# Kernel optimization log

Measured on AMD Instinct MI355X. Metric: run time of the kernel, lower is better.

## Reference

```python
import jax, jax.numpy as jnp
import numpy as np

T, B, F_, H, D, C = 16, 1024, 512, 128, 8, 100  # trees, batch, feat, hidden, depth, classes
L = 2 ** (D + 1)  # n_leaf = 512


def _routing_tables():
    # Static per-leaf routing: node index and branch side at each depth.
    # Derived from compute_mu's gather indices:
    #   node(d, l) = 2^d - 1 + l // 2^(D+1-d);  side(d, l) = (l // 2^(D-d)) % 2
    l = np.arange(L)
    node = np.stack([(2 ** d - 1) + l // (2 ** (D + 1 - d)) for d in range(D + 1)])  # [D+1, L]
    side = np.stack([(l // (2 ** (D - d))) % 2 for d in range(D + 1)])               # [D+1, L]
    return jnp.asarray(node, dtype=jnp.int32), jnp.asarray(side.astype(np.bool_))


def setup_inputs() -> dict:
    key = jax.random.key(0)
    ks = jax.random.split(key, 4)
    return {
        "feat": jax.random.normal(ks[0], (B, F_), jnp.float32),
        "W1": jax.random.normal(ks[1], (T, F_, H), jnp.float32) * 0.05,
        "b1": jnp.zeros((T, H), jnp.float32),
        "W2": jax.random.normal(ks[2], (T, H, L), jnp.float32) * 0.05,
        "b2": jnp.zeros((T, L), jnp.float32),
        "pi": jax.random.uniform(ks[3], (T, L, C), jnp.float32, -2.0, 2.0),
    }


def reference(feat, W1, b1, W2, b2, pi):
    node, side = _routing_tables()
    # Per-tree MLP head (dropout is identity in eval mode).
    h = jax.nn.relu(jnp.einsum('bf,tfh->tbh', feat, W1) + b1[:, None, :])        # [T,B,H]
    p = jax.nn.sigmoid(jnp.einsum('tbh,thl->tbl', h, W2) + b2[:, None, :])       # [T,B,L]
    # compute_mu: product of routing probs along each root->leaf path.
    sel = p[:, :, node]                          # [T,B,D+1,L] gather (static indices)
    route = jnp.where(side, 1.0 - sel, sel)      # left -> p, right -> 1-p
    mu = jnp.prod(route, axis=2)                 # [T,B,L]
    # compute_py_x: mean over leaves then mean over trees of mu @ softmax(pi).
    leaf_p = jax.nn.softmax(pi, axis=-1)         # [T,L,C]
    py_x = jnp.einsum('tbl,tlc->bc', mu, leaf_p) / (L * T)  # [B,C]
    return jnp.log(py_x)
```

## Files before the change

### kernel.cpp

```cpp
#include <hip/hip_runtime.h>
#include <hip/hip_bf16.h>
#include <math.h>

#define T_ 16
#define B_ 1024
#define F_ 512
#define H_ 128
#define D_ 8
#define C_ 100
#define L_ 512
#define CP_ 112

typedef __attribute__((ext_vector_type(8))) short bf16x8_t;
typedef __attribute__((ext_vector_type(4))) float f32x4_t;

__device__ inline ushort f2bf(float x) {
  __hip_bfloat16 b = __float2bfloat16(x);
  return *(ushort*)&b;
}
__device__ inline float bf2f(ushort u) {
  union { unsigned int i; float f; } v;
  v.i = ((unsigned int)u) << 16;
  return v.f;
}

__device__ inline void bar_raw() {
  asm volatile("" ::: "memory");
  __builtin_amdgcn_s_barrier();
  asm volatile("" ::: "memory");
}
__device__ inline void bar_publish_lds() {
  asm volatile("s_waitcnt lgkmcnt(0)" ::: "memory");
  __builtin_amdgcn_s_barrier();
  asm volatile("" ::: "memory");
}

__global__ __launch_bounds__(256) void k_prep(
    const float* __restrict__ feat, const float* __restrict__ W1,
    const float* __restrict__ W2, const float* __restrict__ pi,
    ushort* __restrict__ feat_bf, ushort* __restrict__ W1T,
    ushort* __restrict__ W2T, ushort* __restrict__ lpT) {
  __shared__ ushort ubuf[112 * 48];
  float (*tile)[33] = (float(*)[33])ubuf;
  ushort (*tileT)[48] = (ushort(*)[48])ubuf;
  const int bid = blockIdx.x, tid = threadIdx.x;

  if (bid < 256) {
    int i = (bid * 256 + tid) * 8;
    float4 a = *(const float4*)(feat + i);
    float4 b = *(const float4*)(feat + i + 4);
    bf16x8_t o;
    o[0] = (short)f2bf(a.x); o[1] = (short)f2bf(a.y);
    o[2] = (short)f2bf(a.z); o[3] = (short)f2bf(a.w);
    o[4] = (short)f2bf(b.x); o[5] = (short)f2bf(b.y);
    o[6] = (short)f2bf(b.z); o[7] = (short)f2bf(b.w);
    *(bf16x8_t*)(feat_bf + i) = o;
    return;
  }
  if (bid < 2304) {
    const float* X; ushort* XT; int K, N, kb, nb, s;
    if (bid < 1280) {
      int r = bid - 256;  kb = r & 15; nb = (r >> 4) & 3;  s = r >> 6;
      X = W1; XT = W1T; K = F_; N = H_;
    } else {
      int r = bid - 1280; kb = r & 3;  nb = (r >> 2) & 15; s = r >> 6;
      X = W2; XT = W2T; K = H_; N = L_;
    }
    const int k0 = kb * 32, n0 = nb * 32;
    const int c = tid & 31, r0 = tid >> 5;
    const float* Xs = X + (size_t)s * K * N;
    ushort* XTs = XT + (size_t)s * N * K;
#pragma unroll
    for (int j = 0; j < 4; ++j)
      tile[r0 + 8 * j][c] = Xs[(size_t)(k0 + r0 + 8 * j) * N + n0 + c];
    __syncthreads();
#pragma unroll
    for (int j = 0; j < 4; ++j)
      XTs[(size_t)(n0 + r0 + 8 * j) * K + k0 + c] = f2bf(tile[c][r0 + 8 * j]);
    return;
  }
  {
    int bid2 = bid - 2304;
    int t = bid2 >> 4, l0 = (bid2 & 15) << 5;
    int lane = tid & 63;
#pragma unroll
    for (int p = 0; p < 8; ++p) {
      int rl = p * 4 + (tid >> 6);
      const float* x = pi + (size_t)(t * L_ + l0 + rl) * C_;
      float v0 = (lane < C_) ? x[lane] : -1e30f;
      float v1 = (lane + 64 < C_) ? x[lane + 64] : -1e30f;
      float m = fmaxf(v0, v1);
#pragma unroll
      for (int off = 32; off; off >>= 1) m = fmaxf(m, __shfl_xor(m, off, 64));
      float e0 = __expf(v0 - m);
      float e1 = (lane + 64 < C_) ? __expf(v1 - m) : 0.0f;
      float sm = e0 + e1;
#pragma unroll
      for (int off = 32; off; off >>= 1) sm += __shfl_xor(sm, off, 64);
      float inv = 1.0f / sm;
      if (lane < C_) tileT[lane][rl] = f2bf(e0 * inv);
      int c2 = lane + 64;
      if (c2 < CP_) tileT[c2][rl] = f2bf(c2 < C_ ? e1 * inv : 0.0f);
    }
    __syncthreads();
    ushort* dst = lpT + (size_t)t * CP_ * L_ + l0;
    for (int idx = tid; idx < 448; idx += 256) {
      int c = idx >> 2, ch = (idx & 3) * 8;
      *(bf16x8_t*)(dst + (size_t)c * L_ + ch) = *(const bf16x8_t*)&tileT[c][ch];
    }
  }
}

__global__ __launch_bounds__(512, 4) void k12_mfma(
    const ushort* __restrict__ feat, const ushort* __restrict__ W1T,
    const float* __restrict__ b1, const ushort* __restrict__ W2T,
    const float* __restrict__ b2, const ushort* __restrict__ lpT,
    float* __restrict__ part) {
  __shared__ ushort smem[29696];
  ushort (*h_s)[136] = (ushort(*)[136])smem;
  ushort (*a_s)[72]  = (ushort(*)[72])(smem + 4352);
  ushort (*b_s)[72]  = (ushort(*)[72])(smem + 6656);
  ushort (*w_s)[136] = (ushort(*)[136])(smem + 4352);
  ushort (*p_s)[520] = (ushort(*)[520])(smem + 13056);

  const int bid = blockIdx.x;
  const int t = bid & 15, b0 = (bid >> 4) * 32;
  const int tid = threadIdx.x;
  const int w = tid >> 6, lane = tid & 63, quad = lane >> 4, n = lane & 15;

  const bool doA = tid < 256;
  const int srow = tid >> 3, scol = (tid & 7) * 8;
  const ushort* featp = feat + (size_t)(b0 + srow) * F_ + scol;
  const ushort* w1p   = W1T + ((size_t)t * H_ + srow) * F_ + scol;

  {
    f32x4_t acc[2];
    acc[0] = (f32x4_t){0.f, 0.f, 0.f, 0.f};
    acc[1] = (f32x4_t){0.f, 0.f, 0.f, 0.f};

    bf16x8_t ra[2], rb[2][2];
    if (doA) ra[0] = *(const bf16x8_t*)(featp);
#pragma unroll
    for (int i = 0; i < 2; ++i)
      rb[0][i] = *(const bf16x8_t*)(w1p + (size_t)i * 64 * F_);
    if (doA) *(bf16x8_t*)&a_s[srow][scol] = ra[0];
#pragma unroll
    for (int i = 0; i < 2; ++i)
      *(bf16x8_t*)&b_s[i * 64 + srow][scol] = rb[0][i];
    bar_publish_lds();
    if (doA) ra[1] = *(const bf16x8_t*)(featp + 64);
#pragma unroll
    for (int i = 0; i < 2; ++i)
      rb[1][i] = *(const bf16x8_t*)(w1p + (size_t)i * 64 * F_ + 64);
    if (doA) ra[0] = *(const bf16x8_t*)(featp + 128);
#pragma unroll
    for (int i = 0; i < 2; ++i)
      rb[0][i] = *(const bf16x8_t*)(w1p + (size_t)i * 64 * F_ + 128);

#pragma unroll
    for (int kc = 0; kc < 8; ++kc) {
#pragma unroll
      for (int ks = 0; ks < 64; ks += 32) {
        bf16x8_t af0 = *(const bf16x8_t*)&a_s[n][ks + quad * 8];
        bf16x8_t af1 = *(const bf16x8_t*)&a_s[16 + n][ks + quad * 8];
        bf16x8_t bfr = *(const bf16x8_t*)&b_s[w * 16 + n][ks + quad * 8];
        acc[0] = __builtin_amdgcn_mfma_f32_16x16x32_bf16(af0, bfr, acc[0],
                                                         0, 0, 0);
        acc[1] = __builtin_amdgcn_mfma_f32_16x16x32_bf16(af1, bfr, acc[1],
                                                         0, 0, 0);
      }
      bar_raw();
      if (kc < 7) {
        const int p = (kc + 1) & 1;
        if (doA) *(bf16x8_t*)&a_s[srow][scol] = ra[p];
#pragma unroll
        for (int i = 0; i < 2; ++i)
          *(bf16x8_t*)&b_s[i * 64 + srow][scol] = rb[p][i];
        bar_publish_lds();
        if (kc < 6) {
          if (doA) ra[p] = *(const bf16x8_t*)(featp + (kc + 3) * 64);
#pragma unroll
          for (int i = 0; i < 2; ++i)
            rb[p][i] = *(const bf16x8_t*)(w1p + (size_t)i * 64 * F_ + (kc + 3) * 64);
        }
      }
    }
    float bias = b1[t * H_ + w * 16 + n];
#pragma unroll
    for (int mt = 0; mt < 2; ++mt)
#pragma unroll
      for (int r = 0; r < 4; ++r) {
        int row = mt * 16 + quad * 4 + r;
        float v = acc[mt][r] + bias;
        h_s[row][w * 16 + n] = f2bf(v > 0.f ? v : 0.f);
      }
  }

  {
    const int wrow = tid >> 4, wcol = (tid & 15) * 8;
    const ushort* w2p = W2T + ((size_t)t * L_ + wrow) * H_ + wcol;
    bf16x8_t rw[2][2];
#pragma unroll
    for (int i = 0; i < 2; ++i)
      rw[0][i] = *(const bf16x8_t*)(w2p + (size_t)(i * 32) * H_);
#pragma unroll
    for (int i = 0; i < 2; ++i)
      rw[1][i] = *(const bf16x8_t*)(w2p + (size_t)(64 + i * 32) * H_);
    bar_publish_lds();

    const int mhalf = w >> 2, lhalf = w & 3;
    bf16x8_t af2[4];
#pragma unroll
    for (int ks = 0; ks < 4; ++ks)
      af2[ks] = *(const bf16x8_t*)&h_s[mhalf * 16 + n][ks * 32 + quad * 8];
#pragma unroll
    for (int i = 0; i < 2; ++i)
      *(bf16x8_t*)&w_s[i * 32 + wrow][wcol] = rw[0][i];
    bar_publish_lds();
#pragma unroll
    for (int i = 0; i < 2; ++i)
      rw[0][i] = *(const bf16x8_t*)(w2p + (size_t)(128 + i * 32) * H_);

#pragma unroll
    for (int nc = 0; nc < 8; ++nc) {
      f32x4_t acc = (f32x4_t){0.f, 0.f, 0.f, 0.f};
#pragma unroll
      for (int ks = 0; ks < 4; ++ks) {
        bf16x8_t bfrag = *(const bf16x8_t*)&w_s[lhalf * 16 + n][ks * 32 + quad * 8];
        acc = __builtin_amdgcn_mfma_f32_16x16x32_bf16(af2[ks], bfrag, acc,
                                                      0, 0, 0);
      }
      int l = nc * 64 + lhalf * 16 + n;
      float bias = b2[t * L_ + l];
#pragma unroll
      for (int r = 0; r < 4; ++r) {
        float x = acc[r] + bias;
        p_s[mhalf * 16 + quad * 4 + r][l] = f2bf(1.0f / (1.0f + __expf(-x)));
      }
      bar_raw();
      if (nc < 7) {
        const int p = (nc + 1) & 1;
#pragma unroll
        for (int i = 0; i < 2; ++i)
          *(bf16x8_t*)&w_s[i * 32 + wrow][wcol] = rw[p][i];
        bar_publish_lds();
        if (nc < 6) {
#pragma unroll
          for (int i = 0; i < 2; ++i)
            rw[p][i] = *(const bf16x8_t*)(w2p + (size_t)((nc + 3) * 64 + i * 32) * H_);
        }
      }
    }
  }
  bar_publish_lds();

  bf16x8_t mo[2][2];
#pragma unroll
  for (int pass = 0; pass < 2; ++pass) {
    int unit = pass * 512 + tid;
    int b = unit >> 5;
    int s = unit & 31;
    float P = 1.f;
#pragma unroll
    for (int d = 0; d < 5; ++d) {
      int nd = (1 << d) - 1 + (s >> (5 - d));
      int sd = (s >> (4 - d)) & 1;
      float pv = bf2f(p_s[b][nd]);
      P *= sd ? (1.f - pv) : pv;
    }
    float p5 = bf2f(p_s[b][31 + s]);
    float q5[2] = {P * p5, P * (1.f - p5)};
    float q6[4], q7[8];
#pragma unroll
    for (int j = 0; j < 2; ++j) {
      float pv = bf2f(p_s[b][63 + 2 * s + j]);
      q6[2 * j] = q5[j] * pv;
      q6[2 * j + 1] = q5[j] * (1.f - pv);
    }
#pragma unroll
    for (int u = 0; u < 4; ++u) {
      float pv = bf2f(p_s[b][127 + 4 * s + u]);
      q7[2 * u] = q6[u] * pv;
      q7[2 * u + 1] = q6[u] * (1.f - pv);
    }
    bf16x8_t o0, o1;
#pragma unroll
    for (int v = 0; v < 8; ++v) {
      float pv = bf2f(p_s[b][255 + 8 * s + v]);
      ushort e0 = f2bf(q7[v] * pv);
      ushort e1 = f2bf(q7[v] * (1.f - pv));
      if (v < 4) { o0[2 * v] = (short)e0; o0[2 * v + 1] = (short)e1; }
      else       { o1[2 * (v - 4)] = (short)e0; o1[2 * (v - 4) + 1] = (short)e1; }
    }
    mo[pass][0] = o0;
    mo[pass][1] = o1;
  }
  bar_raw();
#pragma unroll
  for (int pass = 0; pass < 2; ++pass) {
    int unit = pass * 512 + tid;
    int b = unit >> 5;
    int s = unit & 31;
    *(bf16x8_t*)&p_s[b][s * 16]     = mo[pass][0];
    *(bf16x8_t*)&p_s[b][s * 16 + 8] = mo[pass][1];
  }
  bar_publish_lds();

  {
#pragma unroll
    for (int uu = 0; uu < 2; ++uu) {
      int u = w + uu * 8;
      if (u < 14) {
        const int mt = u & 1, nt = u >> 1;
        const ushort* arow = &p_s[mt * 16 + n][0];
        const ushort* brow = lpT + (size_t)t * CP_ * L_ +
                             ((size_t)(nt * 16 + n)) * L_ + quad * 8;
        f32x4_t acc = (f32x4_t){0.f, 0.f, 0.f, 0.f};
#pragma unroll 4
        for (int k = 0; k < L_; k += 32) {
          bf16x8_t af = *(const bf16x8_t*)(arow + k + quad * 8);
          bf16x8_t bfr = *(const bf16x8_t*)(brow + k);
          acc = __builtin_amdgcn_mfma_f32_16x16x32_bf16(af, bfr, acc, 0, 0, 0);
        }
        const int m0 = b0 + mt * 16 + quad * 4;
        const int c = nt * 16 + n;
        if (c < C_) {
#pragma unroll
          for (int r = 0; r < 4; ++r)
            part[((size_t)t * B_ + m0 + r) * C_ + c] = acc[r];
        }
      }
    }
  }
}

__global__ __launch_bounds__(256) void k6_log(
    const float* __restrict__ part, float* __restrict__ out) {
  int i = (blockIdx.x * 256 + threadIdx.x) * 4;
  if (i < B_ * C_) {
    float4 s = {0.f, 0.f, 0.f, 0.f};
#pragma unroll
    for (int t = 0; t < T_; ++t) {
      float4 v = *(const float4*)(part + (size_t)t * B_ * C_ + i);
      s.x += v.x; s.y += v.y; s.z += v.z; s.w += v.w;
    }
    const float inv = 1.0f / (L_ * T_);
    float4 o;
    o.x = logf(s.x * inv); o.y = logf(s.y * inv);
    o.z = logf(s.z * inv); o.w = logf(s.w * inv);
    *(float4*)(out + i) = o;
  }
}

extern "C" void kernel_launch(void* const* d_in, const int* in_sizes, int n_in,
                              void* d_out, int out_size, void* d_ws,
                              size_t ws_size, hipStream_t stream) {
  const float* feat = (const float*)d_in[0];
  const float* W1   = (const float*)d_in[1];
  const float* b1   = (const float*)d_in[2];
  const float* W2   = (const float*)d_in[3];
  const float* b2   = (const float*)d_in[4];
  const float* pi   = (const float*)d_in[5];
  float* out = (float*)d_out;

  char* ws = (char*)d_ws;
  ushort* feat_bf  = (ushort*)(ws);
  ushort* W1T_buf  = (ushort*)(ws + ((size_t)1 << 20));
  ushort* W2T_buf  = (ushort*)(ws + ((size_t)3 << 20));
  ushort* lpT_buf  = (ushort*)(ws + ((size_t)5 << 20));
  float*  part_buf = (float*)(ws + ((size_t)7 << 20));

  k_prep<<<2560, 256, 0, stream>>>(feat, W1, W2, pi, feat_bf, W1T_buf,
                                   W2T_buf, lpT_buf);
  k12_mfma<<<512, 512, 0, stream>>>(feat_bf, W1T_buf, b1, W2T_buf, b2,
                                    lpT_buf, part_buf);
  k6_log<<<(B_ * C_ / 4 + 255) / 256, 256, 0, stream>>>(part_buf, out);
}
```

Measured before the change: 108.4 us.

## Load MFMA B-operands directly from global into registers, fuse feat bf16 cast

The feat fp32-to-bf16 conversion moves out of the prep kernel and into the main kernel, which converts its 32-row feat tile straight into LDS. W1, W2 and leaf-probability fragments are now loaded from global memory directly into registers in MFMA layout with register double-buffering, instead of being staged through LDS with repeated barriers. This removes a global round-trip for feat_bf, many LDS writes and barriers, and lowers LDS use. In exchange, register pressure rises and the global loads are less coalesced per wave.

```diff
diff --git a/kernel.cpp b/kernel.cpp
--- a/kernel.cpp
+++ b/kernel.cpp
@@ -36,34 +36,21 @@
 }
 
 __global__ __launch_bounds__(256) void k_prep(
-    const float* __restrict__ feat, const float* __restrict__ W1,
-    const float* __restrict__ W2, const float* __restrict__ pi,
-    ushort* __restrict__ feat_bf, ushort* __restrict__ W1T,
+    const float* __restrict__ W1, const float* __restrict__ W2,
+    const float* __restrict__ pi, ushort* __restrict__ W1T,
     ushort* __restrict__ W2T, ushort* __restrict__ lpT) {
   __shared__ ushort ubuf[112 * 48];
   float (*tile)[33] = (float(*)[33])ubuf;
   ushort (*tileT)[48] = (ushort(*)[48])ubuf;
   const int bid = blockIdx.x, tid = threadIdx.x;
 
-  if (bid < 256) {
-    int i = (bid * 256 + tid) * 8;
-    float4 a = *(const float4*)(feat + i);
-    float4 b = *(const float4*)(feat + i + 4);
-    bf16x8_t o;
-    o[0] = (short)f2bf(a.x); o[1] = (short)f2bf(a.y);
-    o[2] = (short)f2bf(a.z); o[3] = (short)f2bf(a.w);
-    o[4] = (short)f2bf(b.x); o[5] = (short)f2bf(b.y);
-    o[6] = (short)f2bf(b.z); o[7] = (short)f2bf(b.w);
-    *(bf16x8_t*)(feat_bf + i) = o;
-    return;
-  }
-  if (bid < 2304) {
+  if (bid < 2048) {
     const float* X; ushort* XT; int K, N, kb, nb, s;
-    if (bid < 1280) {
-      int r = bid - 256;  kb = r & 15; nb = (r >> 4) & 3;  s = r >> 6;
+    if (bid < 1024) {
+      int r = bid;         kb = r & 15; nb = (r >> 4) & 3;  s = r >> 6;
       X = W1; XT = W1T; K = F_; N = H_;
     } else {
-      int r = bid - 1280; kb = r & 3;  nb = (r >> 2) & 15; s = r >> 6;
+      int r = bid - 1024;  kb = r & 3;  nb = (r >> 2) & 15; s = r >> 6;
       X = W2; XT = W2T; K = H_; N = L_;
     }
     const int k0 = kb * 32, n0 = nb * 32;
@@ -80,7 +67,7 @@
     return;
   }
   {
-    int bid2 = bid - 2304;
+    int bid2 = bid - 2048;
     int t = bid2 >> 4, l0 = (bid2 & 15) << 5;
     int lane = tid & 63;
 #pragma unroll
@@ -112,143 +99,113 @@
 }
 
 __global__ __launch_bounds__(512, 4) void k12_mfma(
-    const ushort* __restrict__ feat, const ushort* __restrict__ W1T,
+    const float* __restrict__ feat, const ushort* __restrict__ W1T,
     const float* __restrict__ b1, const ushort* __restrict__ W2T,
     const float* __restrict__ b2, const ushort* __restrict__ lpT,
     float* __restrict__ part) {
-  __shared__ ushort smem[29696];
+  __shared__ ushort smem[20992];
   ushort (*h_s)[136] = (ushort(*)[136])smem;
-  ushort (*a_s)[72]  = (ushort(*)[72])(smem + 4352);
-  ushort (*b_s)[72]  = (ushort(*)[72])(smem + 6656);
-  ushort (*w_s)[136] = (ushort(*)[136])(smem + 4352);
-  ushort (*p_s)[520] = (ushort(*)[520])(smem + 13056);
+  ushort (*u_s)[520] = (ushort(*)[520])(smem + 4352);
 
   const int bid = blockIdx.x;
   const int t = bid & 15, b0 = (bid >> 4) * 32;
   const int tid = threadIdx.x;
   const int w = tid >> 6, lane = tid & 63, quad = lane >> 4, n = lane & 15;
 
-  const bool doA = tid < 256;
-  const int srow = tid >> 3, scol = (tid & 7) * 8;
-  const ushort* featp = feat + (size_t)(b0 + srow) * F_ + scol;
-  const ushort* w1p   = W1T + ((size_t)t * H_ + srow) * F_ + scol;
-
   {
+    const ushort* w1row = W1T + ((size_t)t * H_ + w * 16 + n) * F_ + quad * 8;
+    bf16x8_t br[4][2];
+#pragma unroll
+    for (int kc = 0; kc < 4; ++kc)
+#pragma unroll
+      for (int ks = 0; ks < 2; ++ks)
+        br[kc][ks] = *(const bf16x8_t*)(w1row + kc * 64 + ks * 32);
+
+    {
+      const int frow = tid >> 4, fc0 = (tid & 15) * 32;
+      const float* fp = feat + (size_t)(b0 + frow) * F_ + fc0;
+#pragma unroll
+      for (int j = 0; j < 4; ++j) {
+        float4 a = *(const float4*)(fp + j * 8);
+        float4 b = *(const float4*)(fp + j * 8 + 4);
+        bf16x8_t o;
+        o[0] = (short)f2bf(a.x); o[1] = (short)f2bf(a.y);
+        o[2] = (short)f2bf(a.z); o[3] = (short)f2bf(a.w);
+        o[4] = (short)f2bf(b.x); o[5] = (short)f2bf(b.y);
+        o[6] = (short)f2bf(b.z); o[7] = (short)f2bf(b.w);
+        *(bf16x8_t*)&u_s[frow][fc0 + j * 8] = o;
+      }
+    }
+    bar_publish_lds();
+
     f32x4_t acc[2];
     acc[0] = (f32x4_t){0.f, 0.f, 0.f, 0.f};
     acc[1] = (f32x4_t){0.f, 0.f, 0.f, 0.f};
-
-    bf16x8_t ra[2], rb[2][2];
-    if (doA) ra[0] = *(const bf16x8_t*)(featp);
-#pragma unroll
-    for (int i = 0; i < 2; ++i)
-      rb[0][i] = *(const bf16x8_t*)(w1p + (size_t)i * 64 * F_);
-    if (doA) *(bf16x8_t*)&a_s[srow][scol] = ra[0];
-#pragma unroll
-    for (int i = 0; i < 2; ++i)
-      *(bf16x8_t*)&b_s[i * 64 + srow][scol] = rb[0][i];
+#pragma unroll
+    for (int kc = 0; kc < 8; ++kc) {
+#pragma unroll
+      for (int ks2 = 0; ks2 < 2; ++ks2) {
+        const int ko = kc * 64 + ks2 * 32 + quad * 8;
+        bf16x8_t af0 = *(const bf16x8_t*)&u_s[n][ko];
+        bf16x8_t af1 = *(const bf16x8_t*)&u_s[16 + n][ko];
+        acc[0] = __builtin_amdgcn_mfma_f32_16x16x32_bf16(af0, br[kc & 3][ks2],
+                                                         acc[0], 0, 0, 0);
+        acc[1] = __builtin_amdgcn_mfma_f32_16x16x32_bf16(af1, br[kc & 3][ks2],
+                                                         acc[1], 0, 0, 0);
+      }
+      if (kc < 4) {
+#pragma unroll
+        for (int ks = 0; ks < 2; ++ks)
+          br[kc & 3][ks] = *(const bf16x8_t*)(w1row + (kc + 4) * 64 + ks * 32);
+      }
+    }
+    float bias = b1[t * H_ + w * 16 + n];
+#pragma unroll
+    for (int mt = 0; mt < 2; ++mt)
+#pragma unroll
+      for (int r = 0; r < 4; ++r) {
+        float v = acc[mt][r] + bias;
+        h_s[mt * 16 + quad * 4 + r][w * 16 + n] = f2bf(v > 0.f ? v : 0.f);
+      }
+  }
+
+  {
+    const int mhalf = w >> 2, lhalf = w & 3;
+    const ushort* w2row =
+        W2T + ((size_t)t * L_ + lhalf * 16 + n) * H_ + quad * 8;
+    bf16x8_t rw[2][4];
+#pragma unroll
+    for (int ks = 0; ks < 4; ++ks)
+      rw[0][ks] = *(const bf16x8_t*)(w2row + ks * 32);
+#pragma unroll
+    for (int ks = 0; ks < 4; ++ks)
+      rw[1][ks] = *(const bf16x8_t*)(w2row + (size_t)64 * H_ + ks * 32);
     bar_publish_lds();
-    if (doA) ra[1] = *(const bf16x8_t*)(featp + 64);
-#pragma unroll
-    for (int i = 0; i < 2; ++i)
-      rb[1][i] = *(const bf16x8_t*)(w1p + (size_t)i * 64 * F_ + 64);
-    if (doA) ra[0] = *(const bf16x8_t*)(featp + 128);
-#pragma unroll
-    for (int i = 0; i < 2; ++i)
-      rb[0][i] = *(const bf16x8_t*)(w1p + (size_t)i * 64 * F_ + 128);
-
-#pragma unroll
-    for (int kc = 0; kc < 8; ++kc) {
-#pragma unroll
-      for (int ks = 0; ks < 64; ks += 32) {
-        bf16x8_t af0 = *(const bf16x8_t*)&a_s[n][ks + quad * 8];
-        bf16x8_t af1 = *(const bf16x8_t*)&a_s[16 + n][ks + quad * 8];
-        bf16x8_t bfr = *(const bf16x8_t*)&b_s[w * 16 + n][ks + quad * 8];
-        acc[0] = __builtin_amdgcn_mfma_f32_16x16x32_bf16(af0, bfr, acc[0],
-                                                         0, 0, 0);
-        acc[1] = __builtin_amdgcn_mfma_f32_16x16x32_bf16(af1, bfr, acc[1],
-                                                         0, 0, 0);
-      }
-      bar_raw();
-      if (kc < 7) {
-        const int p = (kc + 1) & 1;
-        if (doA) *(bf16x8_t*)&a_s[srow][scol] = ra[p];
-#pragma unroll
-        for (int i = 0; i < 2; ++i)
-          *(bf16x8_t*)&b_s[i * 64 + srow][scol] = rb[p][i];
-        bar_publish_lds();
-        if (kc < 6) {
-          if (doA) ra[p] = *(const bf16x8_t*)(featp + (kc + 3) * 64);
-#pragma unroll
-          for (int i = 0; i < 2; ++i)
-            rb[p][i] = *(const bf16x8_t*)(w1p + (size_t)i * 64 * F_ + (kc + 3) * 64);
-        }
-      }
-    }
-    float bias = b1[t * H_ + w * 16 + n];
-#pragma unroll
-    for (int mt = 0; mt < 2; ++mt)
-#pragma unroll
-      for (int r = 0; r < 4; ++r) {
-        int row = mt * 16 + quad * 4 + r;
-        float v = acc[mt][r] + bias;
-        h_s[row][w * 16 + n] = f2bf(v > 0.f ? v : 0.f);
-      }
-  }
-
-  {
-    const int wrow = tid >> 4, wcol = (tid & 15) * 8;
-    const ushort* w2p = W2T + ((size_t)t * L_ + wrow) * H_ + wcol;
-    bf16x8_t rw[2][2];
-#pragma unroll
-    for (int i = 0; i < 2; ++i)
-      rw[0][i] = *(const bf16x8_t*)(w2p + (size_t)(i * 32) * H_);
-#pragma unroll
-    for (int i = 0; i < 2; ++i)
-      rw[1][i] = *(const bf16x8_t*)(w2p + (size_t)(64 + i * 32) * H_);
-    bar_publish_lds();
-
-    const int mhalf = w >> 2, lhalf = w & 3;
+
     bf16x8_t af2[4];
 #pragma unroll
     for (int ks = 0; ks < 4; ++ks)
       af2[ks] = *(const bf16x8_t*)&h_s[mhalf * 16 + n][ks * 32 + quad * 8];
-#pragma unroll
-    for (int i = 0; i < 2; ++i)
-      *(bf16x8_t*)&w_s[i * 32 + wrow][wcol] = rw[0][i];
-    bar_publish_lds();
-#pragma unroll
-    for (int i = 0; i < 2; ++i)
-      rw[0][i] = *(const bf16x8_t*)(w2p + (size_t)(128 + i * 32) * H_);
 
 #pragma unroll
     for (int nc = 0; nc < 8; ++nc) {
       f32x4_t acc = (f32x4_t){0.f, 0.f, 0.f, 0.f};
 #pragma unroll
-      for (int ks = 0; ks < 4; ++ks) {
-        bf16x8_t bfrag = *(const bf16x8_t*)&w_s[lhalf * 16 + n][ks * 32 + quad * 8];
-        acc = __builtin_amdgcn_mfma_f32_16x16x32_bf16(af2[ks], bfrag, acc,
-                                                      0, 0, 0);
+      for (int ks = 0; ks < 4; ++ks)
+        acc = __builtin_amdgcn_mfma_f32_16x16x32_bf16(af2[ks], rw[nc & 1][ks],
+                                                      acc, 0, 0, 0);
+      if (nc < 6) {
+#pragma unroll
+        for (int ks = 0; ks < 4; ++ks)
+          rw[nc & 1][ks] =
+              *(const bf16x8_t*)(w2row + (size_t)(nc + 2) * 64 * H_ + ks * 32);
       }
       int l = nc * 64 + lhalf * 16 + n;
       float bias = b2[t * L_ + l];
 #pragma unroll
       for (int r = 0; r < 4; ++r) {
         float x = acc[r] + bias;
-        p_s[mhalf * 16 + quad * 4 + r][l] = f2bf(1.0f / (1.0f + __expf(-x)));
-      }
-      bar_raw();
-      if (nc < 7) {
-        const int p = (nc + 1) & 1;
-#pragma unroll
-        for (int i = 0; i < 2; ++i)
-          *(bf16x8_t*)&w_s[i * 32 + wrow][wcol] = rw[p][i];
-        bar_publish_lds();
-        if (nc < 6) {
-#pragma unroll
-          for (int i = 0; i < 2; ++i)
-            rw[p][i] = *(const bf16x8_t*)(w2p + (size_t)((nc + 3) * 64 + i * 32) * H_);
-        }
+        u_s[mhalf * 16 + quad * 4 + r][l] = f2bf(1.0f / (1.0f + __expf(-x)));
       }
     }
   }
@@ -265,28 +222,28 @@
     for (int d = 0; d < 5; ++d) {
       int nd = (1 << d) - 1 + (s >> (5 - d));
       int sd = (s >> (4 - d)) & 1;
-      float pv = bf2f(p_s[b][nd]);
+      float pv = bf2f(u_s[b][nd]);
       P *= sd ? (1.f - pv) : pv;
     }
-    float p5 = bf2f(p_s[b][31 + s]);
+    float p5 = bf2f(u_s[b][31 + s]);
     float q5[2] = {P * p5, P * (1.f - p5)};
     float q6[4], q7[8];
 #pragma unroll
     for (int j = 0; j < 2; ++j) {
-      float pv = bf2f(p_s[b][63 + 2 * s + j]);
+      float pv = bf2f(u_s[b][63 + 2 * s + j]);
       q6[2 * j] = q5[j] * pv;
       q6[2 * j + 1] = q5[j] * (1.f - pv);
     }
 #pragma unroll
     for (int u = 0; u < 4; ++u) {
-      float pv = bf2f(p_s[b][127 + 4 * s + u]);
+      float pv = bf2f(u_s[b][127 + 4 * s + u]);
       q7[2 * u] = q6[u] * pv;
       q7[2 * u + 1] = q6[u] * (1.f - pv);
     }
     bf16x8_t o0, o1;
 #pragma unroll
     for (int v = 0; v < 8; ++v) {
-      float pv = bf2f(p_s[b][255 + 8 * s + v]);
+      float pv = bf2f(u_s[b][255 + 8 * s + v]);
       ushort e0 = f2bf(q7[v] * pv);
       ushort e1 = f2bf(q7[v] * (1.f - pv));
       if (v < 4) { o0[2 * v] = (short)e0; o0[2 * v + 1] = (short)e1; }
@@ -301,8 +258,8 @@
     int unit = pass * 512 + tid;
     int b = unit >> 5;
     int s = unit & 31;
-    *(bf16x8_t*)&p_s[b][s * 16]     = mo[pass][0];
-    *(bf16x8_t*)&p_s[b][s * 16 + 8] = mo[pass][1];
+    *(bf16x8_t*)&u_s[b][s * 16]     = mo[pass][0];
+    *(bf16x8_t*)&u_s[b][s * 16 + 8] = mo[pass][1];
   }
   bar_publish_lds();
 
@@ -312,15 +269,21 @@
       int u = w + uu * 8;
       if (u < 14) {
         const int mt = u & 1, nt = u >> 1;
-        const ushort* arow = &p_s[mt * 16 + n][0];
         const ushort* brow = lpT + (size_t)t * CP_ * L_ +
                              ((size_t)(nt * 16 + n)) * L_ + quad * 8;
+        bf16x8_t bfr[8];
+#pragma unroll
+        for (int kk = 0; kk < 8; ++kk)
+          bfr[kk] = *(const bf16x8_t*)(brow + kk * 32);
+        const ushort* arow = &u_s[mt * 16 + n][0];
         f32x4_t acc = (f32x4_t){0.f, 0.f, 0.f, 0.f};
-#pragma unroll 4
-        for (int k = 0; k < L_; k += 32) {
-          bf16x8_t af = *(const bf16x8_t*)(arow + k + quad * 8);
-          bf16x8_t bfr = *(const bf16x8_t*)(brow + k);
-          acc = __builtin_amdgcn_mfma_f32_16x16x32_bf16(af, bfr, acc, 0, 0, 0);
+#pragma unroll
+        for (int kk = 0; kk < 16; ++kk) {
+          bf16x8_t af = *(const bf16x8_t*)(arow + kk * 32 + quad * 8);
+          acc = __builtin_amdgcn_mfma_f32_16x16x32_bf16(af, bfr[kk & 7], acc,
+                                                        0, 0, 0);
+          if (kk < 8)
+            bfr[kk & 7] = *(const bf16x8_t*)(brow + (kk + 8) * 32);
         }
         const int m0 = b0 + mt * 16 + quad * 4;
         const int c = nt * 16 + n;
@@ -364,15 +327,13 @@
   float* out = (float*)d_out;
 
   char* ws = (char*)d_ws;
-  ushort* feat_bf  = (ushort*)(ws);
-  ushort* W1T_buf  = (ushort*)(ws + ((size_t)1 << 20));
-  ushort* W2T_buf  = (ushort*)(ws + ((size_t)3 << 20));
-  ushort* lpT_buf  = (ushort*)(ws + ((size_t)5 << 20));
-  float*  part_buf = (float*)(ws + ((size_t)7 << 20));
-
-  k_prep<<<2560, 256, 0, stream>>>(feat, W1, W2, pi, feat_bf, W1T_buf,
-                                   W2T_buf, lpT_buf);
-  k12_mfma<<<512, 512, 0, stream>>>(feat_bf, W1T_buf, b1, W2T_buf, b2,
+  ushort* W1T_buf  = (ushort*)(ws);
+  ushort* W2T_buf  = (ushort*)(ws + ((size_t)2 << 20));
+  ushort* lpT_buf  = (ushort*)(ws + ((size_t)4 << 20));
+  float*  part_buf = (float*)(ws + ((size_t)6 << 20));
+
+  k_prep<<<2304, 256, 0, stream>>>(W1, W2, pi, W1T_buf, W2T_buf, lpT_buf);
+  k12_mfma<<<512, 512, 0, stream>>>(feat, W1T_buf, b1, W2T_buf, b2,
                                     lpT_buf, part_buf);
   k6_log<<<(B_ * C_ / 4 + 255) / 256, 256, 0, stream>>>(part_buf, out);
 }
```

New measurement: 121.8 us. 12.3% more time.

## Fuse feat bf16 conversion into GEMM and double-buffer LDS tiles

Applied to the files above, without the earlier changes.

The separate feat fp32-to-bf16 conversion blocks are removed from the prep kernel. The main kernel now loads fp32 feat directly and converts it in registers before staging to LDS. The A/B tiles for the first GEMM and the W2 tiles for the second GEMM are double-buffered in LDS, which removes one barrier per iteration. In exchange, LDS use per block grows from about 59KB to 77KB, which may reduce occupancy, and the kernel reads twice as many feat bytes from global memory.

```diff
diff --git a/kernel.cpp b/kernel.cpp
--- a/kernel.cpp
+++ b/kernel.cpp
@@ -36,34 +36,21 @@
 }
 
 __global__ __launch_bounds__(256) void k_prep(
-    const float* __restrict__ feat, const float* __restrict__ W1,
-    const float* __restrict__ W2, const float* __restrict__ pi,
-    ushort* __restrict__ feat_bf, ushort* __restrict__ W1T,
+    const float* __restrict__ W1, const float* __restrict__ W2,
+    const float* __restrict__ pi, ushort* __restrict__ W1T,
     ushort* __restrict__ W2T, ushort* __restrict__ lpT) {
   __shared__ ushort ubuf[112 * 48];
   float (*tile)[33] = (float(*)[33])ubuf;
   ushort (*tileT)[48] = (ushort(*)[48])ubuf;
   const int bid = blockIdx.x, tid = threadIdx.x;
 
-  if (bid < 256) {
-    int i = (bid * 256 + tid) * 8;
-    float4 a = *(const float4*)(feat + i);
-    float4 b = *(const float4*)(feat + i + 4);
-    bf16x8_t o;
-    o[0] = (short)f2bf(a.x); o[1] = (short)f2bf(a.y);
-    o[2] = (short)f2bf(a.z); o[3] = (short)f2bf(a.w);
-    o[4] = (short)f2bf(b.x); o[5] = (short)f2bf(b.y);
-    o[6] = (short)f2bf(b.z); o[7] = (short)f2bf(b.w);
-    *(bf16x8_t*)(feat_bf + i) = o;
-    return;
-  }
-  if (bid < 2304) {
+  if (bid < 2048) {
     const float* X; ushort* XT; int K, N, kb, nb, s;
-    if (bid < 1280) {
-      int r = bid - 256;  kb = r & 15; nb = (r >> 4) & 3;  s = r >> 6;
+    if (bid < 1024) {
+      int r = bid;         kb = r & 15; nb = (r >> 4) & 3;  s = r >> 6;
       X = W1; XT = W1T; K = F_; N = H_;
     } else {
-      int r = bid - 1280; kb = r & 3;  nb = (r >> 2) & 15; s = r >> 6;
+      int r = bid - 1024;  kb = r & 3;  nb = (r >> 2) & 15; s = r >> 6;
       X = W2; XT = W2T; K = H_; N = L_;
     }
     const int k0 = kb * 32, n0 = nb * 32;
@@ -80,7 +67,7 @@
     return;
   }
   {
-    int bid2 = bid - 2304;
+    int bid2 = bid - 2048;
     int t = bid2 >> 4, l0 = (bid2 & 15) << 5;
     int lane = tid & 63;
 #pragma unroll
@@ -112,73 +99,99 @@
 }
 
 __global__ __launch_bounds__(512, 4) void k12_mfma(
-    const ushort* __restrict__ feat, const ushort* __restrict__ W1T,
+    const float* __restrict__ feat, const ushort* __restrict__ W1T,
     const float* __restrict__ b1, const ushort* __restrict__ W2T,
     const float* __restrict__ b2, const ushort* __restrict__ lpT,
     float* __restrict__ part) {
-  __shared__ ushort smem[29696];
+  __shared__ ushort smem[38400];
   ushort (*h_s)[136] = (ushort(*)[136])smem;
-  ushort (*a_s)[72]  = (ushort(*)[72])(smem + 4352);
-  ushort (*b_s)[72]  = (ushort(*)[72])(smem + 6656);
-  ushort (*w_s)[136] = (ushort(*)[136])(smem + 4352);
-  ushort (*p_s)[520] = (ushort(*)[520])(smem + 13056);
+  ushort (*a_s0)[72] = (ushort(*)[72])(smem + 4352);
+  ushort (*a_s1)[72] = (ushort(*)[72])(smem + 4352 + 2304);
+  ushort (*b_s0)[72] = (ushort(*)[72])(smem + 8960);
+  ushort (*b_s1)[72] = (ushort(*)[72])(smem + 8960 + 9216);
+  ushort (*w_s0)[136] = (ushort(*)[136])(smem + 4352);
+  ushort (*w_s1)[136] = (ushort(*)[136])(smem + 4352 + 8704);
+  ushort (*p_s)[520] = (ushort(*)[520])(smem + 21760);
 
   const int bid = blockIdx.x;
   const int t = bid & 15, b0 = (bid >> 4) * 32;
   const int tid = threadIdx.x;
   const int w = tid >> 6, lane = tid & 63, quad = lane >> 4, n = lane & 15;
 
-  const bool doA = tid < 256;
-  const int srow = tid >> 3, scol = (tid & 7) * 8;
-  const ushort* featp = feat + (size_t)(b0 + srow) * F_ + scol;
-  const ushort* w1p   = W1T + ((size_t)t * H_ + srow) * F_ + scol;
-
   {
+    const bool doA = tid < 256;
+    const int srow = tid >> 3, scol = (tid & 7) * 8;
+    const float*  fp32p = feat + (size_t)(b0 + srow) * F_ + scol;
+    const ushort* w1p   = W1T + ((size_t)t * H_ + srow) * F_ + scol;
+
+    float4 ra[2][2];
+    bf16x8_t rb[2][2];
+
+    if (doA) { ra[0][0] = *(const float4*)(fp32p);
+               ra[0][1] = *(const float4*)(fp32p + 4); }
+#pragma unroll
+    for (int i = 0; i < 2; ++i)
+      rb[0][i] = *(const bf16x8_t*)(w1p + (size_t)i * 64 * F_);
+    if (doA) {
+      bf16x8_t o;
+      o[0] = (short)f2bf(ra[0][0].x); o[1] = (short)f2bf(ra[0][0].y);
+      o[2] = (short)f2bf(ra[0][0].z); o[3] = (short)f2bf(ra[0][0].w);
+      o[4] = (short)f2bf(ra[0][1].x); o[5] = (short)f2bf(ra[0][1].y);
+      o[6] = (short)f2bf(ra[0][1].z); o[7] = (short)f2bf(ra[0][1].w);
+      *(bf16x8_t*)&a_s0[srow][scol] = o;
+    }
+#pragma unroll
+    for (int i = 0; i < 2; ++i)
+      *(bf16x8_t*)&b_s0[i * 64 + srow][scol] = rb[0][i];
+    bar_publish_lds();
+    if (doA) { ra[1][0] = *(const float4*)(fp32p + 64);
+               ra[1][1] = *(const float4*)(fp32p + 68); }
+#pragma unroll
+    for (int i = 0; i < 2; ++i)
+      rb[1][i] = *(const bf16x8_t*)(w1p + (size_t)i * 64 * F_ + 64);
+    if (doA) { ra[0][0] = *(const float4*)(fp32p + 128);
+               ra[0][1] = *(const float4*)(fp32p + 132); }
+#pragma unroll
+    for (int i = 0; i < 2; ++i)
+      rb[0][i] = *(const bf16x8_t*)(w1p + (size_t)i * 64 * F_ + 128);
+
     f32x4_t acc[2];
     acc[0] = (f32x4_t){0.f, 0.f, 0.f, 0.f};
     acc[1] = (f32x4_t){0.f, 0.f, 0.f, 0.f};
-
-    bf16x8_t ra[2], rb[2][2];
-    if (doA) ra[0] = *(const bf16x8_t*)(featp);
-#pragma unroll
-    for (int i = 0; i < 2; ++i)
-      rb[0][i] = *(const bf16x8_t*)(w1p + (size_t)i * 64 * F_);
-    if (doA) *(bf16x8_t*)&a_s[srow][scol] = ra[0];
-#pragma unroll
-    for (int i = 0; i < 2; ++i)
-      *(bf16x8_t*)&b_s[i * 64 + srow][scol] = rb[0][i];
-    bar_publish_lds();
-    if (doA) ra[1] = *(const bf16x8_t*)(featp + 64);
-#pragma unroll
-    for (int i = 0; i < 2; ++i)
-      rb[1][i] = *(const bf16x8_t*)(w1p + (size_t)i * 64 * F_ + 64);
-    if (doA) ra[0] = *(const bf16x8_t*)(featp + 128);
-#pragma unroll
-    for (int i = 0; i < 2; ++i)
-      rb[0][i] = *(const bf16x8_t*)(w1p + (size_t)i * 64 * F_ + 128);
-
 #pragma unroll
     for (int kc = 0; kc < 8; ++kc) {
-#pragma unroll
-      for (int ks = 0; ks < 64; ks += 32) {
-        bf16x8_t af0 = *(const bf16x8_t*)&a_s[n][ks + quad * 8];
-        bf16x8_t af1 = *(const bf16x8_t*)&a_s[16 + n][ks + quad * 8];
-        bf16x8_t bfr = *(const bf16x8_t*)&b_s[w * 16 + n][ks + quad * 8];
+      ushort (*ar)[72] = (kc & 1) ? a_s1 : a_s0;
+      ushort (*br)[72] = (kc & 1) ? b_s1 : b_s0;
+#pragma unroll
+      for (int ks2 = 0; ks2 < 2; ++ks2) {
+        const int ko = ks2 * 32 + quad * 8;
+        bf16x8_t af0 = *(const bf16x8_t*)&ar[n][ko];
+        bf16x8_t af1 = *(const bf16x8_t*)&ar[16 + n][ko];
+        bf16x8_t bfr = *(const bf16x8_t*)&br[w * 16 + n][ko];
         acc[0] = __builtin_amdgcn_mfma_f32_16x16x32_bf16(af0, bfr, acc[0],
                                                          0, 0, 0);
         acc[1] = __builtin_amdgcn_mfma_f32_16x16x32_bf16(af1, bfr, acc[1],
                                                          0, 0, 0);
       }
-      bar_raw();
       if (kc < 7) {
         const int p = (kc + 1) & 1;
-        if (doA) *(bf16x8_t*)&a_s[srow][scol] = ra[p];
+        ushort (*aw)[72] = p ? a_s1 : a_s0;
+        ushort (*bw)[72] = p ? b_s1 : b_s0;
+        if (doA) {
+          bf16x8_t o;
+          o[0] = (short)f2bf(ra[p][0].x); o[1] = (short)f2bf(ra[p][0].y);
+          o[2] = (short)f2bf(ra[p][0].z); o[3] = (short)f2bf(ra[p][0].w);
+          o[4] = (short)f2bf(ra[p][1].x); o[5] = (short)f2bf(ra[p][1].y);
+          o[6] = (short)f2bf(ra[p][1].z); o[7] = (short)f2bf(ra[p][1].w);
+          *(bf16x8_t*)&aw[srow][scol] = o;
+        }
 #pragma unroll
         for (int i = 0; i < 2; ++i)
-          *(bf16x8_t*)&b_s[i * 64 + srow][scol] = rb[p][i];
+          *(bf16x8_t*)&bw[i * 64 + srow][scol] = rb[p][i];
         bar_publish_lds();
         if (kc < 6) {
-          if (doA) ra[p] = *(const bf16x8_t*)(featp + (kc + 3) * 64);
+          if (doA) { ra[p][0] = *(const float4*)(fp32p + (kc + 3) * 64);
+                     ra[p][1] = *(const float4*)(fp32p + (kc + 3) * 64 + 4); }
 #pragma unroll
           for (int i = 0; i < 2; ++i)
             rb[p][i] = *(const bf16x8_t*)(w1p + (size_t)i * 64 * F_ + (kc + 3) * 64);
@@ -190,9 +203,8 @@
     for (int mt = 0; mt < 2; ++mt)
 #pragma unroll
       for (int r = 0; r < 4; ++r) {
-        int row = mt * 16 + quad * 4 + r;
         float v = acc[mt][r] + bias;
-        h_s[row][w * 16 + n] = f2bf(v > 0.f ? v : 0.f);
+        h_s[mt * 16 + quad * 4 + r][w * 16 + n] = f2bf(v > 0.f ? v : 0.f);
       }
   }
 
@@ -215,7 +227,7 @@
       af2[ks] = *(const bf16x8_t*)&h_s[mhalf * 16 + n][ks * 32 + quad * 8];
 #pragma unroll
     for (int i = 0; i < 2; ++i)
-      *(bf16x8_t*)&w_s[i * 32 + wrow][wcol] = rw[0][i];
+      *(bf16x8_t*)&w_s0[i * 32 + wrow][wcol] = rw[0][i];
     bar_publish_lds();
 #pragma unroll
     for (int i = 0; i < 2; ++i)
@@ -223,10 +235,11 @@
 
 #pragma unroll
     for (int nc = 0; nc < 8; ++nc) {
+      ushort (*wr)[136] = (nc & 1) ? w_s1 : w_s0;
       f32x4_t acc = (f32x4_t){0.f, 0.f, 0.f, 0.f};
 #pragma unroll
       for (int ks = 0; ks < 4; ++ks) {
-        bf16x8_t bfrag = *(const bf16x8_t*)&w_s[lhalf * 16 + n][ks * 32 + quad * 8];
+        bf16x8_t bfrag = *(const bf16x8_t*)&wr[lhalf * 16 + n][ks * 32 + quad * 8];
         acc = __builtin_amdgcn_mfma_f32_16x16x32_bf16(af2[ks], bfrag, acc,
                                                       0, 0, 0);
       }
@@ -237,12 +250,12 @@
         float x = acc[r] + bias;
         p_s[mhalf * 16 + quad * 4 + r][l] = f2bf(1.0f / (1.0f + __expf(-x)));
       }
-      bar_raw();
       if (nc < 7) {
         const int p = (nc + 1) & 1;
+        ushort (*ww)[136] = p ? w_s1 : w_s0;
 #pragma unroll
         for (int i = 0; i < 2; ++i)
-          *(bf16x8_t*)&w_s[i * 32 + wrow][wcol] = rw[p][i];
+          *(bf16x8_t*)&ww[i * 32 + wrow][wcol] = rw[p][i];
         bar_publish_lds();
         if (nc < 6) {
 #pragma unroll
@@ -364,15 +377,13 @@
   float* out = (float*)d_out;
 
   char* ws = (char*)d_ws;
-  ushort* feat_bf  = (ushort*)(ws);
-  ushort* W1T_buf  = (ushort*)(ws + ((size_t)1 << 20));
-  ushort* W2T_buf  = (ushort*)(ws + ((size_t)3 << 20));
-  ushort* lpT_buf  = (ushort*)(ws + ((size_t)5 << 20));
-  float*  part_buf = (float*)(ws + ((size_t)7 << 20));
-
-  k_prep<<<2560, 256, 0, stream>>>(feat, W1, W2, pi, feat_bf, W1T_buf,
-                                   W2T_buf, lpT_buf);
-  k12_mfma<<<512, 512, 0, stream>>>(feat_bf, W1T_buf, b1, W2T_buf, b2,
+  ushort* W1T_buf  = (ushort*)(ws);
+  ushort* W2T_buf  = (ushort*)(ws + ((size_t)2 << 20));
+  ushort* lpT_buf  = (ushort*)(ws + ((size_t)4 << 20));
+  float*  part_buf = (float*)(ws + ((size_t)6 << 20));
+
+  k_prep<<<2304, 256, 0, stream>>>(W1, W2, pi, W1T_buf, W2T_buf, lpT_buf);
+  k12_mfma<<<512, 512, 0, stream>>>(feat, W1T_buf, b1, W2T_buf, b2,
                                     lpT_buf, part_buf);
   k6_log<<<(B_ * C_ / 4 + 255) / 256, 256, 0, stream>>>(part_buf, out);
 }
```

Result: no change. 108.5 us (+0.1%).
